# Kernel optimization log

Hardware: AMD Instinct MI355X
Metric: run time of the kernel (lower is better)

Reference implementation:

```python
import jax, jax.numpy as jnp
import numpy as np

N = 50000
NEG_SLOPE = 0.2


def gat_conv(x, src, dst, W, al, ar, b, res=None, activation=None):
    # x: [N, F_in]; W: [F_in, H*D]; al, ar: [H, D]; b: [H*D]
    H, D = al.shape
    h = (x @ W).reshape(-1, H, D)                      # [N, H, D]
    el = jnp.sum(h * al, axis=-1)                      # [N, H]
    er = jnp.sum(h * ar, axis=-1)                      # [N, H]
    e = jax.nn.leaky_relu(el[src] + er[dst], NEG_SLOPE)  # [E, H]
    # edge softmax grouped by destination node
    m = jax.ops.segment_max(e, dst, num_segments=N)    # [N, H]
    ex = jnp.exp(e - m[dst])
    s = jax.ops.segment_sum(ex, dst, num_segments=N)   # [N, H]
    alpha = ex / s[dst]                                # [E, H]
    msg = h[src] * alpha[..., None]                    # [E, H, D]
    out = jax.ops.segment_sum(msg, dst, num_segments=N)  # [N, H, D]
    if res is not None:
        if res is True:  # identity residual (F_in == H*D)
            out = out + x.reshape(-1, H, D)
        else:            # projected residual, res: [F_in, H*D]
            out = out + (x @ res).reshape(-1, H, D)
    out = out + b.reshape(1, H, D)
    if activation is not None:
        out = activation(out)
    return out


def setup_inputs() -> dict:
    key = jax.random.key(0)
    ks = jax.random.split(key, 16)
    E = 800000
    IN, HID, CLS, H = 256, 64, 32, 2
    x = jax.random.normal(ks[0], (N, IN), dtype=jnp.float32)
    edge_src = jax.random.randint(ks[1], (E,), 0, N, dtype=jnp.int32)
    edge_dst = jax.random.randint(ks[2], (E,), 0, N, dtype=jnp.int32)

    def lin(k, fi, fo):
        return jax.random.normal(k, (fi, fo), dtype=jnp.float32) * (1.0 / np.sqrt(fi))

    W0 = lin(ks[3], IN, H * HID)
    al0 = jax.random.normal(ks[4], (H, HID), dtype=jnp.float32) * 0.1
    ar0 = jax.random.normal(ks[5], (H, HID), dtype=jnp.float32) * 0.1
    b0 = jnp.zeros((H * HID,), dtype=jnp.float32)
    W1 = lin(ks[6], H * HID, H * HID)
    al1 = jax.random.normal(ks[7], (H, HID), dtype=jnp.float32) * 0.1
    ar1 = jax.random.normal(ks[8], (H, HID), dtype=jnp.float32) * 0.1
    b1 = jnp.zeros((H * HID,), dtype=jnp.float32)
    W2 = lin(ks[9], H * HID, H * CLS)
    al2 = jax.random.normal(ks[10], (H, CLS), dtype=jnp.float32) * 0.1
    ar2 = jax.random.normal(ks[11], (H, CLS), dtype=jnp.float32) * 0.1
    b2 = jnp.zeros((H * CLS,), dtype=jnp.float32)
    Wres2 = lin(ks[12], H * HID, H * CLS)
    return {"x": x, "edge_src": edge_src, "edge_dst": edge_dst,
            "W0": W0, "al0": al0, "ar0": ar0, "b0": b0,
            "W1": W1, "al1": al1, "ar1": ar1, "b1": b1,
            "W2": W2, "al2": al2, "ar2": ar2, "b2": b2,
            "Wres2": Wres2}


def reference(x, edge_src, edge_dst, W0, al0, ar0, b0, W1, al1, ar1, b1,
              W2, al2, ar2, b2, Wres2):
    elu = jax.nn.elu
    h = gat_conv(x, edge_src, edge_dst, W0, al0, ar0, b0,
                 res=None, activation=elu)
    h = h.reshape(h.shape[0], -1)  # flatten heads: [N, H*D]
    h = gat_conv(h, edge_src, edge_dst, W1, al1, ar1, b1,
                 res=True, activation=elu)  # identity residual
    h = h.reshape(h.shape[0], -1)
    h = gat_conv(h, edge_src, edge_dst, W2, al2, ar2, b2,
                 res=Wres2, activation=None)  # [N, H, CLS]
    logits = h.mean(axis=1)  # mean over heads -> [N, CLS]
    return logits
```

## Files before the change

kernel.cpp:

```cpp
#include <hip/hip_runtime.h>
#include <math.h>


typedef unsigned int uint;
typedef unsigned short ushort;
typedef __attribute__((ext_vector_type(8))) short bf16x8;
typedef __attribute__((ext_vector_type(4))) float f32x4;

#define NBK 196
#define BCAP 4608

__device__ inline uint f2bf(float f) {
    uint u = __float_as_uint(f);
    return (u + 0x7fffu + ((u >> 16) & 1u)) >> 16;
}

__device__ inline uint4 pack8(float4 a, float4 b) {
    return make_uint4(f2bf(a.x) | (f2bf(a.y) << 16), f2bf(a.z) | (f2bf(a.w) << 16),
                      f2bf(b.x) | (f2bf(b.y) << 16), f2bf(b.z) | (f2bf(b.w) << 16));
}

__global__ __launch_bounds__(256) void buildA_k(
    const int* __restrict__ src, const int* __restrict__ dst, int E,
    int* __restrict__ bcur, uint* __restrict__ bdata, int nba,
    const float* __restrict__ W0, const float* __restrict__ W1,
    const float* __restrict__ W2, const float* __restrict__ Wr,
    ushort* __restrict__ Wt0, ushort* __restrict__ Wt1,
    ushort* __restrict__ Wt2cat) {
    __shared__ int lhist[NBK];
    __shared__ int gbase[NBK];
    const int t = threadIdx.x;
    if ((int)blockIdx.x >= nba) {
        int wb = blockIdx.x - nba;
        if (wb < 128) {
            int i = wb * 256 + t;
            int n = i >> 8, k = i & 255;
            Wt0[n * 256 + k] = (ushort)f2bf(W0[k * 128 + n]);
        } else if (wb < 192) {
            int i = (wb - 128) * 256 + t;
            int n = i >> 7, k = i & 127;
            Wt1[n * 128 + k] = (ushort)f2bf(W1[k * 128 + n]);
        } else if (wb < 224) {
            int i = (wb - 192) * 256 + t;
            int n = i >> 7, k = i & 127;
            Wt2cat[n * 128 + k] = (ushort)f2bf(W2[k * 64 + n]);
        } else {
            int i = (wb - 224) * 256 + t;
            int n = i >> 7, k = i & 127;
            Wt2cat[(64 + n) * 128 + k] = (ushort)f2bf(Wr[k * 64 + n]);
        }
        return;
    }
    for (int i = t; i < NBK; i += 256) lhist[i] = 0;
    __syncthreads();
    const int e0 = blockIdx.x * 2048 + t * 8;
    uint payload[8], meta[8];
#pragma unroll
    for (int i = 0; i < 8; ++i) {
        int e = e0 + i;
        if (e < E) {
            int s = src[e], d = dst[e];
            int b = d >> 8;
            int r = atomicAdd(&lhist[b], 1);
            payload[i] = ((uint)s << 8) | (uint)(d & 255);
            meta[i] = ((uint)b << 16) | (uint)r;
        } else {
            meta[i] = 0xffffffffu;
        }
    }
    __syncthreads();
    for (int i = t; i < NBK; i += 256) {
        int c = lhist[i];
        gbase[i] = c ? atomicAdd(&bcur[i], c) : 0;
    }
    __syncthreads();
#pragma unroll
    for (int i = 0; i < 8; ++i) {
        if (meta[i] != 0xffffffffu) {
            int b = meta[i] >> 16;
            int pos = gbase[b] + (int)(meta[i] & 0xffffu);
            if (pos < BCAP) bdata[(size_t)b * BCAP + pos] = payload[i];
        }
    }
}

__device__ void bucketB_body(
    float* smemf, int b, const uint* __restrict__ bdata,
    const int* __restrict__ bcur, int* __restrict__ deg,
    int* __restrict__ offs, int* __restrict__ ssrc, int n,
    int* __restrict__ meta, int* __restrict__ nl0, int* __restrict__ nl1,
    int* __restrict__ nl2) {
    int* lhist = (int*)smemf;
    int* lofs  = lhist + 256;
    int* lcur  = lofs + 256;
    int* stmp  = lcur + 256;
    int* lc    = stmp + 256;
    int* lb    = lc + 3;
    int* sgb   = lb + 3;
    const int t = threadIdx.x;
    const int cnt = min(bcur[b], BCAP);
    int cv = (t < NBK) ? min(bcur[t], BCAP) : 0;
    stmp[t] = cv;
    lhist[t] = 0;
    if (t < 3) lc[t] = 0;
    __syncthreads();
    for (int o = 1; o < 256; o <<= 1) {
        int add = (t >= o) ? stmp[t - o] : 0;
        __syncthreads();
        stmp[t] += add;
        __syncthreads();
    }
    if (t == 0) sgb[0] = b ? stmp[b - 1] : 0;
    __syncthreads();
    const int gb = sgb[0];
    const uint* bd = bdata + (size_t)b * BCAP;
    for (int i = t; i < cnt; i += 256)
        atomicAdd(&lhist[bd[i] & 255], 1);
    __syncthreads();
    int v = lhist[t];
    stmp[t] = v;
    __syncthreads();
    for (int o = 1; o < 256; o <<= 1) {
        int add = (t >= o) ? stmp[t - o] : 0;
        __syncthreads();
        stmp[t] += add;
        __syncthreads();
    }
    lofs[t] = stmp[t] - v;
    lcur[t] = 0;
    __syncthreads();
    int node = b * 256 + t;
    int cls = -1, r = 0;
    if (node < n) {
        deg[node] = v;
        offs[node] = gb + lofs[t];
        cls = (v <= 16) ? 0 : ((v <= 32) ? 1 : 2);
        r = atomicAdd(&lc[cls], 1);
    }
    __syncthreads();
    if (t < 3) lb[t] = lc[t] ? atomicAdd(&meta[t], lc[t]) : 0;
    __syncthreads();
    if (node < n) {
        int* nl = (cls == 0) ? nl0 : ((cls == 1) ? nl1 : nl2);
        nl[lb[cls] + r] = node;
    }
    for (int i = t; i < cnt; i += 256) {
        uint p = bd[i];
        int dl = p & 255;
        int rr = atomicAdd(&lcur[dl], 1);
        ssrc[gb + lofs[dl] + rr] = (int)(p >> 8);
    }
}

template <int K, bool L2MODE, bool AFP32>
__device__ void gemm_body(
    float* smem, const float* __restrict__ Af, const ushort* __restrict__ Ab,
    const ushort* __restrict__ Wt, ushort* __restrict__ Hb,
    float* __restrict__ hres, int nrows,
    const float* __restrict__ al, const float* __restrict__ ar,
    float* __restrict__ el, float* __restrict__ er, int bid) {
    constexpr int AS = 72;
    ushort* As = (ushort*)smem;
    ushort* Ws = (ushort*)smem + 128 * AS;
    float* Cs = smem;
    float* alr = smem + 9216;
    const int tid = threadIdx.x;
    const int w = tid >> 6;
    const int lane = tid & 63;
    const int l15 = lane & 15, quad = lane >> 4;
    const int row0 = bid * 128;
    constexpr int NC = L2MODE ? 64 : 128;

    if (tid < 2 * NC) alr[tid] = (tid < NC) ? al[tid] : ar[tid - NC];

    f32x4 acc[2][8];
#pragma unroll
    for (int m = 0; m < 2; ++m)
#pragma unroll
        for (int i = 0; i < 8; ++i) acc[m][i] = (f32x4){0.f, 0.f, 0.f, 0.f};

    for (int kt = 0; kt < K / 64; ++kt) {
        const int k0 = kt * 64;
        if (AFP32) {
#pragma unroll
            for (int t = 0; t < 8; ++t) {
                int idx = tid + t * 256;
                int r = idx >> 4, c4 = idx & 15;
                float4 v = make_float4(0.f, 0.f, 0.f, 0.f);
                if (row0 + r < nrows)
                    v = *(const float4*)&Af[(size_t)(row0 + r) * K + k0 + c4 * 4];
                ushort4 o;
                o.x = (ushort)f2bf(v.x); o.y = (ushort)f2bf(v.y);
                o.z = (ushort)f2bf(v.z); o.w = (ushort)f2bf(v.w);
                *(ushort4*)&As[r * AS + c4 * 4] = o;
            }
        } else {
#pragma unroll
            for (int t = 0; t < 4; ++t) {
                int idx = tid + t * 256;
                int r = idx >> 3, c8 = idx & 7;
                uint4 v = make_uint4(0, 0, 0, 0);
                if (row0 + r < nrows)
                    v = *(const uint4*)&Ab[(size_t)(row0 + r) * K + k0 + c8 * 8];
                *(uint4*)&As[r * AS + c8 * 8] = v;
            }
        }
#pragma unroll
        for (int t = 0; t < 4; ++t) {
            int idx = tid + t * 256;
            int n = idx >> 3, c8 = idx & 7;
            *(uint4*)&Ws[n * AS + c8 * 8] =
                *(const uint4*)&Wt[(size_t)n * K + k0 + c8 * 8];
        }
        __syncthreads();
#pragma unroll
        for (int ks = 0; ks < 2; ++ks) {
            bf16x8 a0 = *(const bf16x8*)&As[(w * 32 + l15) * AS + ks * 32 + quad * 8];
            bf16x8 a1 = *(const bf16x8*)&As[(w * 32 + 16 + l15) * AS + ks * 32 + quad * 8];
#pragma unroll
            for (int ct = 0; ct < 8; ++ct) {
                bf16x8 bf = *(const bf16x8*)&Ws[(ct * 16 + l15) * AS + ks * 32 + quad * 8];
                acc[0][ct] = __builtin_amdgcn_mfma_f32_16x16x32_bf16(a0, bf, acc[0][ct], 0, 0, 0);
                acc[1][ct] = __builtin_amdgcn_mfma_f32_16x16x32_bf16(a1, bf, acc[1][ct], 0, 0, 0);
            }
        }
        __syncthreads();
    }

#pragma unroll
    for (int h = 0; h < 2; ++h) {
        if ((w >> 1) == h) {
            int wl = w & 1;
#pragma unroll
            for (int m = 0; m < 2; ++m)
#pragma unroll
                for (int ct = 0; ct < 8; ++ct)
#pragma unroll
                    for (int r = 0; r < 4; ++r)
                        Cs[(wl * 32 + m * 16 + quad * 4 + r) * 132 + ct * 16 + l15] =
                            acc[m][ct][r];
        }
        __syncthreads();
        const int rbase = row0 + h * 64;
        if (L2MODE) {
#pragma unroll
            for (int t = 0; t < 2; ++t) {
                int chunk = tid + t * 256;
                int r = chunk >> 3, c8 = chunk & 7;
                int grow = rbase + r;
                if (grow < nrows) {
                    float4 v0 = *(float4*)&Cs[r * 132 + c8 * 8];
                    float4 v1 = *(float4*)&Cs[r * 132 + c8 * 8 + 4];
                    *(uint4*)&Hb[(size_t)grow * 64 + c8 * 8] = pack8(v0, v1);
                }
            }
#pragma unroll
            for (int t = 0; t < 4; ++t) {
                int chunk = tid + t * 256;
                int r = chunk >> 4, c4 = chunk & 15;
                int grow = rbase + r;
                if (grow < nrows)
                    *(float4*)&hres[(size_t)grow * 64 + c4 * 4] =
                        *(float4*)&Cs[r * 132 + 64 + c4 * 4];
            }
        } else {
#pragma unroll
            for (int t = 0; t < 4; ++t) {
                int chunk = tid + t * 256;
                int r = chunk >> 4, c8 = chunk & 15;
                int grow = rbase + r;
                if (grow < nrows) {
                    float4 v0 = *(float4*)&Cs[r * 132 + c8 * 8];
                    float4 v1 = *(float4*)&Cs[r * 132 + c8 * 8 + 4];
                    *(uint4*)&Hb[(size_t)grow * 128 + c8 * 8] = pack8(v0, v1);
                }
            }
        }
        {
            constexpr int HD = L2MODE ? 32 : 64;
            int r = tid >> 2, hh = (tid >> 1) & 1, iser = tid & 1;
            int grow = rbase + r;
            const float* coef = alr + iser * NC + hh * HD;
            const float* crow = Cs + r * 132 + hh * HD;
            float sum = 0.f;
#pragma unroll
            for (int i = 0; i < HD; ++i) sum += crow[i] * coef[i];
            if (grow < nrows) (iser ? er : el)[grow * 2 + hh] = sum;
        }
        __syncthreads();
    }
}

template <int K, bool L2MODE, bool AFP32>
__global__ __launch_bounds__(256) void gemm_m(
    const float* __restrict__ Af, const ushort* __restrict__ Ab,
    const ushort* __restrict__ Wt, ushort* __restrict__ Hb,
    float* __restrict__ hres, int nrows,
    const float* __restrict__ al, const float* __restrict__ ar,
    float* __restrict__ el, float* __restrict__ er) {
    __shared__ float smem[9472];
    gemm_body<K, L2MODE, AFP32>(smem, Af, Ab, Wt, Hb, hres, nrows, al, ar,
                                el, er, blockIdx.x);
}

__global__ __launch_bounds__(256) void gemm0_bucketB_k(
    const float* __restrict__ x, const ushort* __restrict__ Wt0,
    ushort* __restrict__ Hb, int nrows,
    const float* __restrict__ al, const float* __restrict__ ar,
    float* __restrict__ el, float* __restrict__ er, int gblk,
    const uint* __restrict__ bdata, const int* __restrict__ bcur,
    int* __restrict__ deg, int* __restrict__ offs, int* __restrict__ ssrc,
    int* __restrict__ meta, int* __restrict__ nl0, int* __restrict__ nl1,
    int* __restrict__ nl2) {
    __shared__ float smem[9472];
    if ((int)blockIdx.x < gblk) {
        gemm_body<256, false, true>(smem, x, nullptr, Wt0, Hb, nullptr, nrows,
                                    al, ar, el, er, blockIdx.x);
    } else {
        bucketB_body(smem, blockIdx.x - gblk, bdata, bcur, deg, offs, ssrc,
                     nrows, meta, nl0, nl1, nl2);
    }
}

template <int D, bool MEAN_HEADS, bool RES_BF16, int LPN>
__device__ __forceinline__ void agg_group(
    int node, int lane, float2* __restrict__ wlsw,
    const int* __restrict__ ssrc, const int* __restrict__ offs,
    const int* __restrict__ deg, const ushort* __restrict__ hb,
    const float* __restrict__ el, const float* __restrict__ er,
    const float* __restrict__ bias, const void* __restrict__ res,
    float* __restrict__ out, ushort* __restrict__ outb, int act) {
    constexpr int F = 2 * D;
    constexpr int CH = F / 8;
    constexpr int ESL = LPN / CH;
    constexpr int UB = 8;
    static_assert(ESL >= 1, "LPN must cover a full row");
    const int g = lane / LPN, sl = lane % LPN;
    const bool valid = node >= 0;
    float2* wls = wlsw + g * (LPN * 2);
    int off = 0, dg = 0;
    float2 ern = make_float2(0.f, 0.f);
    if (valid) {
        off = offs[node];
        dg = deg[node];
        ern = *(const float2*)&er[node * 2];
    }
    const uint4* __restrict__ hp = (const uint4*)hb;
    const int c = sl & (CH - 1);
    const int es = sl / CH;
    const int h1 = (c >= CH / 2) ? 1 : 0;
    const float2* wbase = wls + es * 2 + h1;
    float acc[8];
#pragma unroll
    for (int i = 0; i < 8; ++i) acc[i] = 0.f;

    auto inner = [&](int cnt) {
        for (int p = 0; p < cnt; p += UB * ESL) {
            float2 mw[UB];
#pragma unroll
            for (int u = 0; u < UB; ++u) mw[u] = wbase[(p + u * ESL) * 2];
            uint4 q[UB];
#pragma unroll
            for (int u = 0; u < UB; ++u)
                q[u] = hp[(size_t)__float_as_int(mw[u].x) * CH + c];
#pragma unroll
            for (int u = 0; u < UB; ++u) {
                float wj = mw[u].y;
                acc[0] += wj * __uint_as_float(q[u].x << 16);
                acc[1] += wj * __uint_as_float(q[u].x & 0xffff0000u);
                acc[2] += wj * __uint_as_float(q[u].y << 16);
                acc[3] += wj * __uint_as_float(q[u].y & 0xffff0000u);
                acc[4] += wj * __uint_as_float(q[u].z << 16);
                acc[5] += wj * __uint_as_float(q[u].z & 0xffff0000u);
                acc[6] += wj * __uint_as_float(q[u].w << 16);
                acc[7] += wj * __uint_as_float(q[u].w & 0xffff0000u);
            }
        }
    };

    bool big = false;
    if constexpr (LPN == 64) big = (dg > 64);

    if (!big) {
        int sidx = 0;
        float a = -INFINITY, b = -INFINITY;
        if (valid && sl < dg) {
            sidx = ssrc[off + sl];
            float2 ev = *(const float2*)&el[sidx * 2];
            a = ev.x + ern.x; a = fmaxf(a, 0.2f * a);
            b = ev.y + ern.y; b = fmaxf(b, 0.2f * b);
        }
        float m0 = a, m1 = b;
#pragma unroll
        for (int o = LPN / 2; o; o >>= 1) {
            m0 = fmaxf(m0, __shfl_xor(m0, o));
            m1 = fmaxf(m1, __shfl_xor(m1, o));
        }
        float p0 = (valid && sl < dg) ? __expf(a - m0) : 0.f;
        float p1 = (valid && sl < dg) ? __expf(b - m1) : 0.f;
        float s0 = p0, s1 = p1;
#pragma unroll
        for (int o = LPN / 2; o; o >>= 1) {
            s0 += __shfl_xor(s0, o);
            s1 += __shfl_xor(s1, o);
        }
        float is0 = s0 > 0.f ? 1.f / s0 : 0.f;
        float is1 = s1 > 0.f ? 1.f / s1 : 0.f;
        wls[sl * 2 + 0] = make_float2(__int_as_float(sidx), p0 * is0);
        wls[sl * 2 + 1] = make_float2(__int_as_float(sidx), p1 * is1);
        inner(dg);
    } else if constexpr (LPN == 64) {
        float s0 = 0.f, s1 = 0.f;
        float m0 = -INFINITY, m1 = -INFINITY;
        for (int k = sl; k < dg; k += 64) {
            int sidx = ssrc[off + k];
            float2 ev = *(const float2*)&el[sidx * 2];
            float a = ev.x + ern.x; a = fmaxf(a, 0.2f * a);
            float b = ev.y + ern.y; b = fmaxf(b, 0.2f * b);
            float nm = fmaxf(m0, a);
            s0 = s0 * __expf(m0 - nm) + __expf(a - nm); m0 = nm;
            nm = fmaxf(m1, b);
            s1 = s1 * __expf(m1 - nm) + __expf(b - nm); m1 = nm;
        }
        for (int o = 32; o; o >>= 1) {
            float om = __shfl_xor(m0, o), os = __shfl_xor(s0, o);
            float nm = fmaxf(m0, om);
            s0 = (nm == -INFINITY) ? 0.f : s0 * __expf(m0 - nm) + os * __expf(om - nm);
            m0 = nm;
            om = __shfl_xor(m1, o); os = __shfl_xor(s1, o);
            nm = fmaxf(m1, om);
            s1 = (nm == -INFINITY) ? 0.f : s1 * __expf(m1 - nm) + os * __expf(om - nm);
            m1 = nm;
        }
        float is0 = s0 > 0.f ? 1.f / s0 : 0.f;
        float is1 = s1 > 0.f ? 1.f / s1 : 0.f;
        for (int cc = 0; cc < dg; cc += 64) {
            int k = cc + sl;
            int sidx = 0;
            float w0 = 0.f, w1 = 0.f;
            if (k < dg) {
                sidx = ssrc[off + k];
                float2 ev = *(const float2*)&el[sidx * 2];
                float a = ev.x + ern.x; a = fmaxf(a, 0.2f * a);
                float b = ev.y + ern.y; b = fmaxf(b, 0.2f * b);
                w0 = __expf(a - m0) * is0;
                w1 = __expf(b - m1) * is1;
            }
            wls[sl * 2 + 0] = make_float2(__int_as_float(sidx), w0);
            wls[sl * 2 + 1] = make_float2(__int_as_float(sidx), w1);
            inner(min(64, dg - cc));
        }
    }

#pragma unroll
    for (int o = CH; o < LPN; o <<= 1) {
#pragma unroll
        for (int i = 0; i < 8; ++i) acc[i] += __shfl_xor(acc[i], o);
    }
    if (!valid) return;

    const int f0 = c * 8;
    float4 b0v = *(const float4*)&bias[f0];
    float4 b1v = *(const float4*)&bias[f0 + 4];
    float vv[8] = {acc[0] + b0v.x, acc[1] + b0v.y, acc[2] + b0v.z, acc[3] + b0v.w,
                   acc[4] + b1v.x, acc[5] + b1v.y, acc[6] + b1v.z, acc[7] + b1v.w};
    if (res) {
        if (RES_BF16) {
            uint4 r = ((const uint4*)res)[(size_t)node * CH + c];
            vv[0] += __uint_as_float(r.x << 16);
            vv[1] += __uint_as_float(r.x & 0xffff0000u);
            vv[2] += __uint_as_float(r.y << 16);
            vv[3] += __uint_as_float(r.y & 0xffff0000u);
            vv[4] += __uint_as_float(r.z << 16);
            vv[5] += __uint_as_float(r.z & 0xffff0000u);
            vv[6] += __uint_as_float(r.w << 16);
            vv[7] += __uint_as_float(r.w & 0xffff0000u);
        } else {
            const float* rf = (const float*)res;
            float4 r0v = *(const float4*)&rf[(size_t)node * F + f0];
            float4 r1v = *(const float4*)&rf[(size_t)node * F + f0 + 4];
            vv[0] += r0v.x; vv[1] += r0v.y; vv[2] += r0v.z; vv[3] += r0v.w;
            vv[4] += r1v.x; vv[5] += r1v.y; vv[6] += r1v.z; vv[7] += r1v.w;
        }
    }
    if (act) {
#pragma unroll
        for (int i = 0; i < 8; ++i)
            vv[i] = vv[i] > 0.f ? vv[i] : __expf(vv[i]) - 1.f;
    }
    if (MEAN_HEADS) {
        float ov[8];
#pragma unroll
        for (int i = 0; i < 8; ++i) ov[i] = __shfl_xor(vv[i], CH / 2);
        if (es == 0 && c < CH / 2) {
            float4 u0 = make_float4(0.5f * (vv[0] + ov[0]), 0.5f * (vv[1] + ov[1]),
                                    0.5f * (vv[2] + ov[2]), 0.5f * (vv[3] + ov[3]));
            float4 u1 = make_float4(0.5f * (vv[4] + ov[4]), 0.5f * (vv[5] + ov[5]),
                                    0.5f * (vv[6] + ov[6]), 0.5f * (vv[7] + ov[7]));
            *(float4*)&out[(size_t)node * D + f0] = u0;
            *(float4*)&out[(size_t)node * D + f0 + 4] = u1;
        }
    } else if (es == 0) {
        if (out) {
            *(float4*)&out[(size_t)node * F + f0] =
                make_float4(vv[0], vv[1], vv[2], vv[3]);
            *(float4*)&out[(size_t)node * F + f0 + 4] =
                make_float4(vv[4], vv[5], vv[6], vv[7]);
        }
        if (outb) {
            *(uint4*)&outb[(size_t)node * F + f0] =
                pack8(make_float4(vv[0], vv[1], vv[2], vv[3]),
                      make_float4(vv[4], vv[5], vv[6], vv[7]));
        }
    }
}

template <int D, bool MEAN_HEADS, bool RES_BF16>
__global__ __launch_bounds__(256) void agg_c2(
    const int* __restrict__ meta, const int* __restrict__ nl0,
    const int* __restrict__ nl1, const int* __restrict__ nl2,
    const int* __restrict__ ssrc, const int* __restrict__ offs,
    const int* __restrict__ deg, const ushort* __restrict__ hb,
    const float* __restrict__ el, const float* __restrict__ er,
    const float* __restrict__ bias, const void* __restrict__ res,
    float* __restrict__ out, ushort* __restrict__ outb, int act) {
    __shared__ float2 wls_all[4][128];
    const int wid = threadIdx.x >> 6;
    const int lane = threadIdx.x & 63;
    float2* wls = wls_all[wid];
    const int c0 = meta[0], c1 = meta[1], c2 = meta[2];
    const int I0 = (c0 + 3) >> 2;
    const int I01 = I0 + ((c1 + 1) >> 1);
    const int T = I01 + c2;
    const int nW = gridDim.x * 4;
    for (int it = blockIdx.x * 4 + wid; it < T; it += nW) {
        if (it < I0) {
            int idx = it * 4 + (lane >> 4);
            int node = (idx < c0) ? nl0[idx] : -1;
            agg_group<D, MEAN_HEADS, RES_BF16, 16>(node, lane, wls, ssrc, offs,
                                                   deg, hb, el, er, bias, res,
                                                   out, outb, act);
        } else if (it < I01) {
            int idx = (it - I0) * 2 + (lane >> 5);
            int node = (idx < c1) ? nl1[idx] : -1;
            agg_group<D, MEAN_HEADS, RES_BF16, 32>(node, lane, wls, ssrc, offs,
                                                   deg, hb, el, er, bias, res,
                                                   out, outb, act);
        } else {
            int node = nl2[it - I01];
            agg_group<D, MEAN_HEADS, RES_BF16, 64>(node, lane, wls, ssrc, offs,
                                                   deg, hb, el, er, bias, res,
                                                   out, outb, act);
        }
    }
}


extern "C" void kernel_launch(void* const* d_in, const int* in_sizes, int n_in,
                              void* d_out, int out_size, void* d_ws, size_t ws_size,
                              hipStream_t stream) {
    const float* x     = (const float*)d_in[0];
    const int*   esrc  = (const int*)d_in[1];
    const int*   edst  = (const int*)d_in[2];
    const float* W0    = (const float*)d_in[3];
    const float* al0   = (const float*)d_in[4];
    const float* ar0   = (const float*)d_in[5];
    const float* b0    = (const float*)d_in[6];
    const float* W1    = (const float*)d_in[7];
    const float* al1   = (const float*)d_in[8];
    const float* ar1   = (const float*)d_in[9];
    const float* b1    = (const float*)d_in[10];
    const float* W2    = (const float*)d_in[11];
    const float* al2   = (const float*)d_in[12];
    const float* ar2   = (const float*)d_in[13];
    const float* b2    = (const float*)d_in[14];
    const float* Wres2 = (const float*)d_in[15];

    const int N = in_sizes[0] / 256;
    const int E = in_sizes[1];

    float* ws = (float*)d_ws;
    float* hres  = ws;
    float* el    = hres + (size_t)N * 64;
    float* er    = el + (size_t)N * 2;
    int* deg     = (int*)(er + (size_t)N * 2);
    int* offs    = deg + N;
    int* bcur    = offs + N;
    int* bbase   = bcur + 256;
    int* ssrc    = bbase + 256;
    uint* bdata  = (uint*)(ssrc + E);
    ushort* Hb   = (ushort*)(bdata + (size_t)NBK * BCAP);
    ushort* Ab   = Hb + (size_t)N * 128;
    ushort* Bb   = Ab + (size_t)N * 128;
    ushort* Wt0  = Bb + (size_t)N * 128;
    ushort* Wt1  = Wt0 + 128 * 256;
    ushort* Wt2c = Wt1 + 128 * 128;
    int* nl0     = (int*)(Wt2c + 128 * 128);
    int* nl1     = nl0 + N;
    int* nl2     = nl1 + N;
    int* meta    = bcur + 208;

    hipMemsetAsync(bcur, 0, 256 * sizeof(int), stream);
    const int nba = (E + 2047) / 2048;
    buildA_k<<<nba + 256, 256, 0, stream>>>(esrc, edst, E, bcur, bdata, nba,
                                            W0, W1, W2, Wres2, Wt0, Wt1, Wt2c);

    const int gblk = (N + 127) / 128;
    const int ablk = 2048;

    gemm0_bucketB_k<<<gblk + NBK, 256, 0, stream>>>(
        x, Wt0, Hb, N, al0, ar0, el, er, gblk,
        bdata, bcur, deg, offs, ssrc, meta, nl0, nl1, nl2);
    agg_c2<64, false, false><<<ablk, 256, 0, stream>>>(
        meta, nl0, nl1, nl2, ssrc, offs, deg, Hb, el, er, b0, nullptr,
        nullptr, Ab, 1);

    gemm_m<128, false, false><<<gblk, 256, 0, stream>>>(
        nullptr, Ab, Wt1, Hb, nullptr, N, al1, ar1, el, er);
    agg_c2<64, false, true><<<ablk, 256, 0, stream>>>(
        meta, nl0, nl1, nl2, ssrc, offs, deg, Hb, el, er, b1, Ab,
        nullptr, Bb, 1);

    gemm_m<128, true, false><<<gblk, 256, 0, stream>>>(
        nullptr, Bb, Wt2c, Hb, hres, N, al2, ar2, el, er);
    agg_c2<32, true, false><<<ablk, 256, 0, stream>>>(
        meta, nl0, nl1, nl2, ssrc, offs, deg, Hb, el, er, b2, hres,
        (float*)d_out, nullptr, 0);
}
```

Measured before the change: 274.2 us.

## Load A fragments directly from global into registers with 64-row GEMM tiles

```diff
diff --git a/kernel.cpp b/kernel.cpp
--- a/kernel.cpp
+++ b/kernel.cpp
@@ -159,135 +159,129 @@
     float* __restrict__ hres, int nrows,
     const float* __restrict__ al, const float* __restrict__ ar,
     float* __restrict__ el, float* __restrict__ er, int bid) {
-    constexpr int AS = 72;
-    ushort* As = (ushort*)smem;
-    ushort* Ws = (ushort*)smem + 128 * AS;
+    constexpr int WS = 136;
+    ushort* Ws = (ushort*)smem;
     float* Cs = smem;
-    float* alr = smem + 9216;
+    float* alr = smem + 8704;
     const int tid = threadIdx.x;
     const int w = tid >> 6;
     const int lane = tid & 63;
     const int l15 = lane & 15, quad = lane >> 4;
-    const int row0 = bid * 128;
+    const int w2 = w >> 1;
+    const int wc = w & 1;
+    const int row0 = bid * 64;
     constexpr int NC = L2MODE ? 64 : 128;
 
     if (tid < 2 * NC) alr[tid] = (tid < NC) ? al[tid] : ar[tid - NC];
 
-    f32x4 acc[2][8];
+    const int ar0i = row0 + w2 * 32 + l15;
+    const bool av0 = ar0i < nrows;
+    const bool av1 = ar0i + 16 < nrows;
+
+    f32x4 acc[2][4];
 #pragma unroll
     for (int m = 0; m < 2; ++m)
 #pragma unroll
-        for (int i = 0; i < 8; ++i) acc[m][i] = (f32x4){0.f, 0.f, 0.f, 0.f};
-
-    for (int kt = 0; kt < K / 64; ++kt) {
-        const int k0 = kt * 64;
-        if (AFP32) {
-#pragma unroll
-            for (int t = 0; t < 8; ++t) {
-                int idx = tid + t * 256;
-                int r = idx >> 4, c4 = idx & 15;
-                float4 v = make_float4(0.f, 0.f, 0.f, 0.f);
-                if (row0 + r < nrows)
-                    v = *(const float4*)&Af[(size_t)(row0 + r) * K + k0 + c4 * 4];
-                ushort4 o;
-                o.x = (ushort)f2bf(v.x); o.y = (ushort)f2bf(v.y);
-                o.z = (ushort)f2bf(v.z); o.w = (ushort)f2bf(v.w);
-                *(ushort4*)&As[r * AS + c4 * 4] = o;
+        for (int i = 0; i < 4; ++i) acc[m][i] = (f32x4){0.f, 0.f, 0.f, 0.f};
+
+    union BC { uint4 u; bf16x8 b; };
+
+#pragma unroll
+    for (int kh = 0; kh < K / 128; ++kh) {
+        if (kh) __syncthreads();
+#pragma unroll
+        for (int t = 0; t < 8; ++t) {
+            int idx = tid + t * 256;
+            int n = idx >> 4, c8 = idx & 15;
+            *(uint4*)&Ws[n * WS + c8 * 8] =
+                *(const uint4*)&Wt[(size_t)n * K + kh * 128 + c8 * 8];
+        }
+        __syncthreads();
+#pragma unroll
+        for (int ks = 0; ks < 4; ++ks) {
+            const int kc = kh * 128 + ks * 32 + quad * 8;
+            bf16x8 af0 = {0, 0, 0, 0, 0, 0, 0, 0};
+            bf16x8 af1 = {0, 0, 0, 0, 0, 0, 0, 0};
+            if (AFP32) {
+                if (av0) {
+                    float4 v0 = *(const float4*)&Af[(size_t)ar0i * K + kc];
+                    float4 v1 = *(const float4*)&Af[(size_t)ar0i * K + kc + 4];
+                    BC cu; cu.u = pack8(v0, v1); af0 = cu.b;
+                }
+                if (av1) {
+                    float4 v0 = *(const float4*)&Af[(size_t)(ar0i + 16) * K + kc];
+                    float4 v1 = *(const float4*)&Af[(size_t)(ar0i + 16) * K + kc + 4];
+                    BC cu; cu.u = pack8(v0, v1); af1 = cu.b;
+                }
+            } else {
+                if (av0) af0 = *(const bf16x8*)&Ab[(size_t)ar0i * K + kc];
+                if (av1) af1 = *(const bf16x8*)&Ab[(size_t)(ar0i + 16) * K + kc];
             }
-        } else {
-#pragma unroll
-            for (int t = 0; t < 4; ++t) {
-                int idx = tid + t * 256;
-                int r = idx >> 3, c8 = idx & 7;
-                uint4 v = make_uint4(0, 0, 0, 0);
-                if (row0 + r < nrows)
-                    v = *(const uint4*)&Ab[(size_t)(row0 + r) * K + k0 + c8 * 8];
-                *(uint4*)&As[r * AS + c8 * 8] = v;
+#pragma unroll
+            for (int ct = 0; ct < 4; ++ct) {
+                bf16x8 bf = *(const bf16x8*)&Ws[(wc * 64 + ct * 16 + l15) * WS +
+                                                ks * 32 + quad * 8];
+                acc[0][ct] = __builtin_amdgcn_mfma_f32_16x16x32_bf16(af0, bf, acc[0][ct], 0, 0, 0);
+                acc[1][ct] = __builtin_amdgcn_mfma_f32_16x16x32_bf16(af1, bf, acc[1][ct], 0, 0, 0);
             }
         }
+    }
+    __syncthreads();
+
+#pragma unroll
+    for (int m = 0; m < 2; ++m)
+#pragma unroll
+        for (int ct = 0; ct < 4; ++ct)
+#pragma unroll
+            for (int r = 0; r < 4; ++r)
+                Cs[(w2 * 32 + m * 16 + quad * 4 + r) * 132 +
+                   wc * 64 + ct * 16 + l15] = acc[m][ct][r];
+    __syncthreads();
+
+    if (L2MODE) {
+#pragma unroll
+        for (int t = 0; t < 2; ++t) {
+            int chunk = tid + t * 256;
+            int r = chunk >> 3, c8 = chunk & 7;
+            int grow = row0 + r;
+            if (grow < nrows) {
+                float4 v0 = *(float4*)&Cs[r * 132 + c8 * 8];
+                float4 v1 = *(float4*)&Cs[r * 132 + c8 * 8 + 4];
+                *(uint4*)&Hb[(size_t)grow * 64 + c8 * 8] = pack8(v0, v1);
+            }
+        }
 #pragma unroll
         for (int t = 0; t < 4; ++t) {
-            int idx = tid + t * 256;
-            int n = idx >> 3, c8 = idx & 7;
-            *(uint4*)&Ws[n * AS + c8 * 8] =
-                *(const uint4*)&Wt[(size_t)n * K + k0 + c8 * 8];
-        }
-        __syncthreads();
-#pragma unroll
-        for (int ks = 0; ks < 2; ++ks) {
-            bf16x8 a0 = *(const bf16x8*)&As[(w * 32 + l15) * AS + ks * 32 + quad * 8];
-            bf16x8 a1 = *(const bf16x8*)&As[(w * 32 + 16 + l15) * AS + ks * 32 + quad * 8];
-#pragma unroll
-            for (int ct = 0; ct < 8; ++ct) {
-                bf16x8 bf = *(const bf16x8*)&Ws[(ct * 16 + l15) * AS + ks * 32 + quad * 8];
-                acc[0][ct] = __builtin_amdgcn_mfma_f32_16x16x32_bf16(a0, bf, acc[0][ct], 0, 0, 0);
-                acc[1][ct] = __builtin_amdgcn_mfma_f32_16x16x32_bf16(a1, bf, acc[1][ct], 0, 0, 0);
+            int chunk = tid + t * 256;
+            int r = chunk >> 4, c4 = chunk & 15;
+            int grow = row0 + r;
+            if (grow < nrows)
+                *(float4*)&hres[(size_t)grow * 64 + c4 * 4] =
+                    *(float4*)&Cs[r * 132 + 64 + c4 * 4];
+        }
+    } else {
+#pragma unroll
+        for (int t = 0; t < 4; ++t) {
+            int chunk = tid + t * 256;
+            int r = chunk >> 4, c8 = chunk & 15;
+            int grow = row0 + r;
+            if (grow < nrows) {
+                float4 v0 = *(float4*)&Cs[r * 132 + c8 * 8];
+                float4 v1 = *(float4*)&Cs[r * 132 + c8 * 8 + 4];
+                *(uint4*)&Hb[(size_t)grow * 128 + c8 * 8] = pack8(v0, v1);
             }
         }
-        __syncthreads();
-    }
-
-#pragma unroll
-    for (int h = 0; h < 2; ++h) {
-        if ((w >> 1) == h) {
-            int wl = w & 1;
-#pragma unroll
-            for (int m = 0; m < 2; ++m)
-#pragma unroll
-                for (int ct = 0; ct < 8; ++ct)
-#pragma unroll
-                    for (int r = 0; r < 4; ++r)
-                        Cs[(wl * 32 + m * 16 + quad * 4 + r) * 132 + ct * 16 + l15] =
-                            acc[m][ct][r];
-        }
-        __syncthreads();
-        const int rbase = row0 + h * 64;
-        if (L2MODE) {
-#pragma unroll
-            for (int t = 0; t < 2; ++t) {
-                int chunk = tid + t * 256;
-                int r = chunk >> 3, c8 = chunk & 7;
-                int grow = rbase + r;
-                if (grow < nrows) {
-                    float4 v0 = *(float4*)&Cs[r * 132 + c8 * 8];
-                    float4 v1 = *(float4*)&Cs[r * 132 + c8 * 8 + 4];
-                    *(uint4*)&Hb[(size_t)grow * 64 + c8 * 8] = pack8(v0, v1);
-                }
-            }
-#pragma unroll
-            for (int t = 0; t < 4; ++t) {
-                int chunk = tid + t * 256;
-                int r = chunk >> 4, c4 = chunk & 15;
-                int grow = rbase + r;
-                if (grow < nrows)
-                    *(float4*)&hres[(size_t)grow * 64 + c4 * 4] =
-                        *(float4*)&Cs[r * 132 + 64 + c4 * 4];
-            }
-        } else {
-#pragma unroll
-            for (int t = 0; t < 4; ++t) {
-                int chunk = tid + t * 256;
-                int r = chunk >> 4, c8 = chunk & 15;
-                int grow = rbase + r;
-                if (grow < nrows) {
-                    float4 v0 = *(float4*)&Cs[r * 132 + c8 * 8];
-                    float4 v1 = *(float4*)&Cs[r * 132 + c8 * 8 + 4];
-                    *(uint4*)&Hb[(size_t)grow * 128 + c8 * 8] = pack8(v0, v1);
-                }
-            }
-        }
-        {
-            constexpr int HD = L2MODE ? 32 : 64;
-            int r = tid >> 2, hh = (tid >> 1) & 1, iser = tid & 1;
-            int grow = rbase + r;
-            const float* coef = alr + iser * NC + hh * HD;
-            const float* crow = Cs + r * 132 + hh * HD;
-            float sum = 0.f;
-#pragma unroll
-            for (int i = 0; i < HD; ++i) sum += crow[i] * coef[i];
-            if (grow < nrows) (iser ? er : el)[grow * 2 + hh] = sum;
-        }
-        __syncthreads();
+    }
+    {
+        constexpr int HD = L2MODE ? 32 : 64;
+        int r = tid >> 2, hh = (tid >> 1) & 1, iser = tid & 1;
+        int grow = row0 + r;
+        const float* coef = alr + iser * NC + hh * HD;
+        const float* crow = Cs + r * 132 + hh * HD;
+        float sum = 0.f;
+#pragma unroll
+        for (int i = 0; i < HD; ++i) sum += crow[i] * coef[i];
+        if (grow < nrows) (iser ? er : el)[grow * 2 + hh] = sum;
     }
 }
 
@@ -298,7 +292,7 @@
     float* __restrict__ hres, int nrows,
     const float* __restrict__ al, const float* __restrict__ ar,
     float* __restrict__ el, float* __restrict__ er) {
-    __shared__ float smem[9472];
+    __shared__ float smem[8960];
     gemm_body<K, L2MODE, AFP32>(smem, Af, Ab, Wt, Hb, hres, nrows, al, ar,
                                 el, er, blockIdx.x);
 }
@@ -312,7 +306,7 @@
     int* __restrict__ deg, int* __restrict__ offs, int* __restrict__ ssrc,
     int* __restrict__ meta, int* __restrict__ nl0, int* __restrict__ nl1,
     int* __restrict__ nl2) {
-    __shared__ float smem[9472];
+    __shared__ float smem[8960];
     if ((int)blockIdx.x < gblk) {
         gemm_body<256, false, true>(smem, x, nullptr, Wt0, Hb, nullptr, nrows,
                                     al, ar, el, er, blockIdx.x);
@@ -605,7 +599,7 @@
     buildA_k<<<nba + 256, 256, 0, stream>>>(esrc, edst, E, bcur, bdata, nba,
                                             W0, W1, W2, Wres2, Wt0, Wt1, Wt2c);
 
-    const int gblk = (N + 127) / 128;
+    const int gblk = (N + 63) / 64;
     const int ablk = 2048;
 
     gemm0_bucketB_k<<<gblk + NBK, 256, 0, stream>>>(
```

Result: faster. 265.2 us (median of 2 runs) (-3.3%).
